# Kernel optimization log

Hardware: AMD Instinct MI355X
Metric: run time of the kernel (lower is better)

Reference implementation:

```python
import jax, jax.numpy as jnp
import numpy as np

PAD_H, PAD_W = 13, 17  # padded grid
GRID_H, GRID_W = 11, 15  # real hex grid (165 hexes)


def _build_convinds() -> np.ndarray:
    """Flat indices into the (13*17,) padded grid of the 7 hex neighbors per cell."""
    off0 = np.array([-17, -16, -1, 0, 1, 17, 18])
    off1 = np.array([-18, -17, -1, 0, 1, 16, 17])
    inds = np.zeros((GRID_H, GRID_W, 7), dtype=np.int32)
    for y in range(1, GRID_H + 1):
        for x in range(1, GRID_W + 1):
            base = y * PAD_W + x
            inds[y - 1, x - 1] = (off0 if y % 2 == 0 else off1) + base
    return inds.reshape(-1)  # (165*7,)


def setup_inputs() -> dict:
    key = jax.random.key(0)
    k1, k2, k3 = jax.random.split(key, 3)
    B, HEXDIM, OUT = 2048, 64, 64
    x = jax.random.normal(k1, (B, 165, HEXDIM), dtype=jnp.float32)
    W = jax.random.normal(k2, (OUT, 7 * HEXDIM), dtype=jnp.float32) * 0.05
    bias = jax.random.normal(k3, (OUT,), dtype=jnp.float32) * 0.05
    return {"x": x, "W": W, "bias": bias}


def reference(x, W, bias):
    convinds = jnp.asarray(_build_convinds())  # static (1155,)
    b, _, hexdim = x.shape
    xg = x.reshape(b, GRID_H, GRID_W, hexdim)
    padded = jnp.zeros((b, PAD_H, PAD_W, hexdim), dtype=x.dtype)
    padded = padded.at[:, 1:GRID_H + 1, 1:GRID_W + 1, :].set(xg)
    padded = padded.reshape(b, PAD_H * PAD_W, hexdim)
    # gather 7 neighbors per hex -> (b, 165, 7*hexdim)
    fc_in = padded[:, convinds, :].reshape(b, 165, 7 * hexdim)
    return jnp.einsum('bnk,ok->bno', fc_in, W) + bias
```

## Files before the change

kernel.cpp:

```cpp
#include <hip/hip_runtime.h>
#include <stdint.h>

typedef __bf16 bf16x8 __attribute__((ext_vector_type(8)));
typedef float floatx4 __attribute__((ext_vector_type(4)));
typedef uint32_t uint32x4 __attribute__((ext_vector_type(4)));

#define GRID_W   15
#define PAD_W    17
#define CELLS    221
#define HEXDIM   64
#define NHEX     165
#define OUTC     64
#define KDIM     448
#define CWORDS   32
#define SXWORDS  (CELLS * CWORDS)
#define SPB      4
#define XF4      (NHEX * HEXDIM / 4)

__device__ __forceinline__ uint32_t pack2bf(float a, float b) {
    union { float f; uint32_t u; } ua, ub;
    ua.f = a; ub.f = b;
    uint32_t ra = (ua.u + 0x7fffu + ((ua.u >> 16) & 1u)) >> 16;
    uint32_t rb = (ub.u + 0x7fffu + ((ub.u >> 16) & 1u)) >> 16;
    return ra | (rb << 16);
}

__global__ void wprep_kernel(const float* __restrict__ W, uint32_t* __restrict__ Wbf) {
    int i = blockIdx.x * 256 + threadIdx.x;
    float4 v = ((const float4*)W)[i];
    uint2 p; p.x = pack2bf(v.x, v.y); p.y = pack2bf(v.z, v.w);
    ((uint2*)Wbf)[i] = p;
}

__device__ __forceinline__ floatx4 mfma16(uint32x4 a, uint32x4 b, floatx4 c) {
    return __builtin_amdgcn_mfma_f32_16x16x32_bf16(
        __builtin_bit_cast(bf16x8, a), __builtin_bit_cast(bf16x8, b), c, 0, 0, 0);
}

template<int HALF>
__device__ __forceinline__ void compute_half(const uint32_t* __restrict__ sb,
                                             const uint32_t* __restrict__ w0,
                                             const uint32_t* __restrict__ w1,
                                             const int* base3, const int* use3,
                                             const int* valid3, int kq, int mg,
                                             floatx4 acc[3][2])
{
    const int off0[7] = {-17, -16, -1, 0, 1, 17, 18};
    const int off1[7] = {-18, -17, -1, 0, 1, 16, 17};
    #pragma unroll
    for (int ksl = 0; ksl < 7; ++ksl) {
        uint32x4 wfa = *(const uint32x4*)(w0 + HALF * 112 + ksl * 16);
        uint32x4 wfb = *(const uint32x4*)(w1 + HALF * 112 + ksl * 16);
        const int ks = HALF * 7 + ksl;
        const int j  = ks >> 1;
        const int h  = ks & 1;
        #pragma unroll
        for (int mt3 = 0; mt3 < 3; ++mt3) {
            if ((mg * 3 + mt3) * 16 < NHEX) {
                int c  = valid3[mt3] ? (base3[mt3] + (use3[mt3] ? off0[j] : off1[j]))
                                     : 16;
                int ch = ((h * 4 + kq) ^ (c & 7));
                uint32x4 bv = *(const uint32x4*)(sb + c * CWORDS + ch * 4);
                acc[mt3][0] = mfma16(wfa, bv, acc[mt3][0]);
                acc[mt3][1] = mfma16(wfb, bv, acc[mt3][1]);
            }
        }
    }
}

__global__ __launch_bounds__(512, 2)
void hexconv_kernel(const float* __restrict__ x,
                    const uint32_t* __restrict__ Wbf,
                    const float* __restrict__ bias,
                    float* __restrict__ out, int B)
{
    __shared__ __align__(16) uint32_t sx[2 * SXWORDS];

    const int tid  = threadIdx.x;
    const int wave = tid >> 6;
    const int lane = tid & 63;
    const int col  = lane & 15;
    const int kq   = lane >> 4;
    const int og   = wave & 1;
    const int mg   = wave >> 1;

    const uint32_t* w0 = Wbf + (og * 32 + col) * (KDIM / 2) + kq * 4;
    const uint32_t* w1 = w0 + 16 * (KDIM / 2);

    int dstoff[6];
    #pragma unroll
    for (int j = 0; j < 6; ++j) {
        int i  = tid + j * 512;
        int ii = (i < XF4) ? i : 0;
        int n = ii >> 4, d = ii & 15;
        int y0 = n / GRID_W, x0 = n - y0 * GRID_W;
        int cell = (y0 + 1) * PAD_W + (x0 + 1);
        int pc   = (d >> 1) ^ (cell & 7);
        dstoff[j] = cell * CWORDS + pc * 4 + (d & 1) * 2;
    }

    const int s0 = blockIdx.x * SPB;
    const float4* xs0 = (const float4*)x + (size_t)s0 * XF4;

    {
        float4 pv[6];
        if (s0 < B) {
            #pragma unroll
            for (int j = 0; j < 5; ++j) pv[j] = xs0[tid + j * 512];
            if (tid < XF4 - 5 * 512) pv[5] = xs0[tid + 5 * 512];
        }
        if (tid < 56 * 8) {
            int c = tid >> 3, ch = tid & 7;
            int cell;
            if (c < 17)      cell = c;
            else if (c < 34) cell = 12 * PAD_W + (c - 17);
            else if (c < 45) cell = (c - 33) * PAD_W;
            else             cell = (c - 44) * PAD_W + 16;
            uint32x4 z = {0u, 0u, 0u, 0u};
            *(uint32x4*)(sx + cell * CWORDS + ch * 4) = z;
            *(uint32x4*)(sx + SXWORDS + cell * CWORDS + ch * 4) = z;
        }
        if (s0 < B) {
            #pragma unroll
            for (int j = 0; j < 5; ++j) {
                uint2 p; p.x = pack2bf(pv[j].x, pv[j].y); p.y = pack2bf(pv[j].z, pv[j].w);
                *(uint2*)(sx + dstoff[j]) = p;
            }
            if (tid < XF4 - 5 * 512) {
                uint2 p; p.x = pack2bf(pv[5].x, pv[5].y); p.y = pack2bf(pv[5].z, pv[5].w);
                *(uint2*)(sx + dstoff[5]) = p;
            }
        }
    }
    __syncthreads();

    #pragma unroll 1
    for (int s = 0; s < SPB; ++s) {
        const int  gs   = s0 + s;
        const bool sval = gs < B;
        const bool nval = (s + 1 < SPB) && (gs + 1 < B);
        const uint32_t* sb = sx + (s & 1) * SXWORDS;

        int base3[3], use3[3], valid3[3];
        floatx4 acc[3][2];
        #pragma unroll
        for (int m = 0; m < 3; ++m) {
            acc[m][0] = (floatx4){0.f, 0.f, 0.f, 0.f};
            acc[m][1] = (floatx4){0.f, 0.f, 0.f, 0.f};
        }

        if (sval) {
            #pragma unroll
            for (int mt3 = 0; mt3 < 3; ++mt3) {
                int mt = mg * 3 + mt3;
                int n  = mt * 16 + col;
                bool valid = (n < NHEX);
                int nn = valid ? n : 0;
                int y0 = nn / GRID_W, x0 = nn - y0 * GRID_W;
                base3[mt3]  = (y0 + 1) * PAD_W + (x0 + 1);
                use3[mt3]   = (y0 & 1);
                valid3[mt3] = valid;
            }
            compute_half<0>(sb, w0, w1, base3, use3, valid3, kq, mg, acc);
        }

        float4 sv[6];
        if (nval) {
            __builtin_amdgcn_sched_barrier(0);
            const float4* xsn = xs0 + (size_t)(s + 1) * XF4;
            #pragma unroll
            for (int j = 0; j < 5; ++j) sv[j] = xsn[tid + j * 512];
            if (tid < XF4 - 5 * 512) sv[5] = xsn[tid + 5 * 512];
            __builtin_amdgcn_sched_barrier(0);
        }

        if (sval) compute_half<1>(sb, w0, w1, base3, use3, valid3, kq, mg, acc);

        if (s + 1 < SPB) {
            if (nval) {
                uint32_t* db = sx + ((s + 1) & 1) * SXWORDS;
                #pragma unroll
                for (int j = 0; j < 5; ++j) {
                    uint2 p; p.x = pack2bf(sv[j].x, sv[j].y); p.y = pack2bf(sv[j].z, sv[j].w);
                    *(uint2*)(db + dstoff[j]) = p;
                }
                if (tid < XF4 - 5 * 512) {
                    uint2 p; p.x = pack2bf(sv[5].x, sv[5].y); p.y = pack2bf(sv[5].z, sv[5].w);
                    *(uint2*)(db + dstoff[5]) = p;
                }
            }
            __syncthreads();
        }

        if (sval) {
            float4 b40 = *(const float4*)(bias + og * 32 + kq * 4);
            float4 b41 = *(const float4*)(bias + og * 32 + 16 + kq * 4);
            float* outb = out + (size_t)gs * NHEX * OUTC;
            #pragma unroll
            for (int mt3 = 0; mt3 < 3; ++mt3) {
                int n = (mg * 3 + mt3) * 16 + col;
                if (n < NHEX) {
                    float* po = outb + (size_t)n * OUTC + og * 32 + kq * 4;
                    float4 v0, v1;
                    v0.x = acc[mt3][0][0] + b40.x; v0.y = acc[mt3][0][1] + b40.y;
                    v0.z = acc[mt3][0][2] + b40.z; v0.w = acc[mt3][0][3] + b40.w;
                    v1.x = acc[mt3][1][0] + b41.x; v1.y = acc[mt3][1][1] + b41.y;
                    v1.z = acc[mt3][1][2] + b41.z; v1.w = acc[mt3][1][3] + b41.w;
                    *(float4*)po        = v0;
                    *(float4*)(po + 16) = v1;
                }
            }
        }
    }
}

extern "C" void kernel_launch(void* const* d_in, const int* in_sizes, int n_in,
                              void* d_out, int out_size, void* d_ws, size_t ws_size,
                              hipStream_t stream) {
    const float* x    = (const float*)d_in[0];
    const float* W    = (const float*)d_in[1];
    const float* bias = (const float*)d_in[2];
    float* out        = (float*)d_out;
    uint32_t* Wbf     = (uint32_t*)d_ws;

    wprep_kernel<<<28, 256, 0, stream>>>(W, Wbf);

    int B = in_sizes[0] / (NHEX * HEXDIM);
    int nb = (B + SPB - 1) / SPB;
    hexconv_kernel<<<nb, 512, 0, stream>>>(x, Wbf, bias, out, B);
}
```

Measured before the change: 210.6 us.

## Pipeline hex conv over half-channel units with padded smem stride

Splits each sample's 64 input channels into two 32-channel halves that are staged and double-buffered separately in LDS, using a padded cell stride of 20 words instead of an XOR swizzle over 32. The weights are reordered in the prep kernel to match the half-channel K ordering. Samples per block drop from 4 to 2, giving twice as many blocks. Smaller LDS buffers and finer-grained units are meant to raise occupancy and overlap global loads with MFMA work, at the cost of more barriers per sample.

```diff
diff --git a/kernel.cpp b/kernel.cpp
--- a/kernel.cpp
+++ b/kernel.cpp
@@ -12,10 +12,11 @@
 #define NHEX     165
 #define OUTC     64
 #define KDIM     448
-#define CWORDS   32
-#define SXWORDS  (CELLS * CWORDS)
-#define SPB      4
-#define XF4      (NHEX * HEXDIM / 4)
+#define CSTRIDE  20
+#define HBWORDS  (CELLS * CSTRIDE)
+#define SPB      2
+#define NUNITS   (2 * SPB)
+#define HF4      (NHEX * 8)
 
 __device__ __forceinline__ uint32_t pack2bf(float a, float b) {
     union { float f; uint32_t u; } ua, ub;
@@ -26,46 +27,19 @@
 }
 
 __global__ void wprep_kernel(const float* __restrict__ W, uint32_t* __restrict__ Wbf) {
-    int i = blockIdx.x * 256 + threadIdx.x;
-    float4 v = ((const float4*)W)[i];
-    uint2 p; p.x = pack2bf(v.x, v.y); p.y = pack2bf(v.z, v.w);
-    ((uint2*)Wbf)[i] = p;
+    int o = blockIdx.x;
+    int r = threadIdx.x;
+    if (r < 224) {
+        int H = r / 112, rr = r - H * 112;
+        int j = rr >> 4, w = rr & 15;
+        const float* src = W + o * KDIM + j * 64 + H * 32 + w * 2;
+        Wbf[o * 224 + r] = pack2bf(src[0], src[1]);
+    }
 }
 
 __device__ __forceinline__ floatx4 mfma16(uint32x4 a, uint32x4 b, floatx4 c) {
     return __builtin_amdgcn_mfma_f32_16x16x32_bf16(
         __builtin_bit_cast(bf16x8, a), __builtin_bit_cast(bf16x8, b), c, 0, 0, 0);
-}
-
-template<int HALF>
-__device__ __forceinline__ void compute_half(const uint32_t* __restrict__ sb,
-                                             const uint32_t* __restrict__ w0,
-                                             const uint32_t* __restrict__ w1,
-                                             const int* base3, const int* use3,
-                                             const int* valid3, int kq, int mg,
-                                             floatx4 acc[3][2])
-{
-    const int off0[7] = {-17, -16, -1, 0, 1, 17, 18};
-    const int off1[7] = {-18, -17, -1, 0, 1, 16, 17};
-    #pragma unroll
-    for (int ksl = 0; ksl < 7; ++ksl) {
-        uint32x4 wfa = *(const uint32x4*)(w0 + HALF * 112 + ksl * 16);
-        uint32x4 wfb = *(const uint32x4*)(w1 + HALF * 112 + ksl * 16);
-        const int ks = HALF * 7 + ksl;
-        const int j  = ks >> 1;
-        const int h  = ks & 1;
-        #pragma unroll
-        for (int mt3 = 0; mt3 < 3; ++mt3) {
-            if ((mg * 3 + mt3) * 16 < NHEX) {
-                int c  = valid3[mt3] ? (base3[mt3] + (use3[mt3] ? off0[j] : off1[j]))
-                                     : 16;
-                int ch = ((h * 4 + kq) ^ (c & 7));
-                uint32x4 bv = *(const uint32x4*)(sb + c * CWORDS + ch * 4);
-                acc[mt3][0] = mfma16(wfa, bv, acc[mt3][0]);
-                acc[mt3][1] = mfma16(wfb, bv, acc[mt3][1]);
-            }
-        }
-    }
 }
 
 __global__ __launch_bounds__(512, 2)
@@ -74,7 +48,7 @@
                     const float* __restrict__ bias,
                     float* __restrict__ out, int B)
 {
-    __shared__ __align__(16) uint32_t sx[2 * SXWORDS];
+    __shared__ __align__(16) uint32_t sx[2 * HBWORDS];
 
     const int tid  = threadIdx.x;
     const int wave = tid >> 6;
@@ -84,130 +58,148 @@
     const int og   = wave & 1;
     const int mg   = wave >> 1;
 
-    const uint32_t* w0 = Wbf + (og * 32 + col) * (KDIM / 2) + kq * 4;
-    const uint32_t* w1 = w0 + 16 * (KDIM / 2);
-
-    int dstoff[6];
+    const uint32_t* w0 = Wbf + (og * 32 + col) * 224 + kq * 4;
+    const uint32_t* w1 = w0 + 16 * 224;
+
+    int soff[3], doff[3];
     #pragma unroll
-    for (int j = 0; j < 6; ++j) {
+    for (int j = 0; j < 3; ++j) {
         int i  = tid + j * 512;
-        int ii = (i < XF4) ? i : 0;
-        int n = ii >> 4, d = ii & 15;
+        int ii = (i < HF4) ? i : 0;
+        int n = ii >> 3, dh = ii & 7;
         int y0 = n / GRID_W, x0 = n - y0 * GRID_W;
         int cell = (y0 + 1) * PAD_W + (x0 + 1);
-        int pc   = (d >> 1) ^ (cell & 7);
-        dstoff[j] = cell * CWORDS + pc * 4 + (d & 1) * 2;
+        soff[j] = n * 16 + dh;
+        doff[j] = cell * CSTRIDE + dh * 2;
+    }
+    const bool v2 = tid < (HF4 - 2 * 512);
+
+    const int off0[7] = {-17, -16, -1, 0, 1, 17, 18};
+    const int off1[7] = {-18, -17, -1, 0, 1, 16, 17};
+    int base3[3], use3[3], valid3[3];
+    #pragma unroll
+    for (int mt3 = 0; mt3 < 3; ++mt3) {
+        int n = (mg * 3 + mt3) * 16 + col;
+        bool valid = (n < NHEX);
+        int nn = valid ? n : 0;
+        int y0 = nn / GRID_W, x0 = nn - y0 * GRID_W;
+        base3[mt3]  = (y0 + 1) * PAD_W + (x0 + 1);
+        use3[mt3]   = (y0 & 1);
+        valid3[mt3] = valid;
     }
 
     const int s0 = blockIdx.x * SPB;
-    const float4* xs0 = (const float4*)x + (size_t)s0 * XF4;
+    const float4* xb = (const float4*)(x + (size_t)s0 * NHEX * HEXDIM);
 
     {
-        float4 pv[6];
+        float4 pv0, pv1, pv2;
         if (s0 < B) {
-            #pragma unroll
-            for (int j = 0; j < 5; ++j) pv[j] = xs0[tid + j * 512];
-            if (tid < XF4 - 5 * 512) pv[5] = xs0[tid + 5 * 512];
-        }
-        if (tid < 56 * 8) {
-            int c = tid >> 3, ch = tid & 7;
+            pv0 = xb[soff[0]];
+            pv1 = xb[soff[1]];
+            if (v2) pv2 = xb[soff[2]];
+        }
+        if (tid < 448) {
+            int t = tid; int buf = t >= 224; t -= buf * 224;
+            int c = t >> 2, ch = t & 3;
             int cell;
             if (c < 17)      cell = c;
             else if (c < 34) cell = 12 * PAD_W + (c - 17);
             else if (c < 45) cell = (c - 33) * PAD_W;
             else             cell = (c - 44) * PAD_W + 16;
             uint32x4 z = {0u, 0u, 0u, 0u};
-            *(uint32x4*)(sx + cell * CWORDS + ch * 4) = z;
-            *(uint32x4*)(sx + SXWORDS + cell * CWORDS + ch * 4) = z;
+            *(uint32x4*)(sx + buf * HBWORDS + cell * CSTRIDE + ch * 4) = z;
         }
         if (s0 < B) {
+            uint2 p;
+            p.x = pack2bf(pv0.x, pv0.y); p.y = pack2bf(pv0.z, pv0.w);
+            *(uint2*)(sx + doff[0]) = p;
+            p.x = pack2bf(pv1.x, pv1.y); p.y = pack2bf(pv1.z, pv1.w);
+            *(uint2*)(sx + doff[1]) = p;
+            if (v2) {
+                p.x = pack2bf(pv2.x, pv2.y); p.y = pack2bf(pv2.z, pv2.w);
+                *(uint2*)(sx + doff[2]) = p;
+            }
+        }
+    }
+    __syncthreads();
+
+    floatx4 acc[3][2];
+    #pragma unroll 1
+    for (int u = 0; u < NUNITS; ++u) {
+        const int s = u >> 1, H = u & 1;
+        const bool uval = (s0 + s) < B;
+        const bool nval = (u + 1 < NUNITS) && ((s0 + ((u + 1) >> 1)) < B);
+        const uint32_t* sb = sx + H * HBWORDS;
+
+        if (H == 0) {
             #pragma unroll
-            for (int j = 0; j < 5; ++j) {
-                uint2 p; p.x = pack2bf(pv[j].x, pv[j].y); p.y = pack2bf(pv[j].z, pv[j].w);
-                *(uint2*)(sx + dstoff[j]) = p;
-            }
-            if (tid < XF4 - 5 * 512) {
-                uint2 p; p.x = pack2bf(pv[5].x, pv[5].y); p.y = pack2bf(pv[5].z, pv[5].w);
-                *(uint2*)(sx + dstoff[5]) = p;
-            }
-        }
-    }
-    __syncthreads();
-
-    #pragma unroll 1
-    for (int s = 0; s < SPB; ++s) {
-        const int  gs   = s0 + s;
-        const bool sval = gs < B;
-        const bool nval = (s + 1 < SPB) && (gs + 1 < B);
-        const uint32_t* sb = sx + (s & 1) * SXWORDS;
-
-        int base3[3], use3[3], valid3[3];
-        floatx4 acc[3][2];
-        #pragma unroll
-        for (int m = 0; m < 3; ++m) {
-            acc[m][0] = (floatx4){0.f, 0.f, 0.f, 0.f};
-            acc[m][1] = (floatx4){0.f, 0.f, 0.f, 0.f};
-        }
-
-        if (sval) {
+            for (int m = 0; m < 3; ++m) {
+                acc[m][0] = (floatx4){0.f, 0.f, 0.f, 0.f};
+                acc[m][1] = (floatx4){0.f, 0.f, 0.f, 0.f};
+            }
+        }
+
+        float4 sv0, sv1, sv2;
+        if (nval) {
+            const float4* xs = xb + (size_t)((u + 1) >> 1) * (NHEX * HEXDIM / 4);
+            int hb = ((u + 1) & 1) * 8;
+            sv0 = xs[soff[0] + hb];
+            sv1 = xs[soff[1] + hb];
+            if (v2) sv2 = xs[soff[2] + hb];
+            __builtin_amdgcn_sched_barrier(0);
+        }
+
+        if (uval) {
+            const int Hw = H * 112;
             #pragma unroll
-            for (int mt3 = 0; mt3 < 3; ++mt3) {
-                int mt = mg * 3 + mt3;
-                int n  = mt * 16 + col;
-                bool valid = (n < NHEX);
-                int nn = valid ? n : 0;
-                int y0 = nn / GRID_W, x0 = nn - y0 * GRID_W;
-                base3[mt3]  = (y0 + 1) * PAD_W + (x0 + 1);
-                use3[mt3]   = (y0 & 1);
-                valid3[mt3] = valid;
-            }
-            compute_half<0>(sb, w0, w1, base3, use3, valid3, kq, mg, acc);
-        }
-
-        float4 sv[6];
-        if (nval) {
-            __builtin_amdgcn_sched_barrier(0);
-            const float4* xsn = xs0 + (size_t)(s + 1) * XF4;
-            #pragma unroll
-            for (int j = 0; j < 5; ++j) sv[j] = xsn[tid + j * 512];
-            if (tid < XF4 - 5 * 512) sv[5] = xsn[tid + 5 * 512];
-            __builtin_amdgcn_sched_barrier(0);
-        }
-
-        if (sval) compute_half<1>(sb, w0, w1, base3, use3, valid3, kq, mg, acc);
-
-        if (s + 1 < SPB) {
+            for (int j = 0; j < 7; ++j) {
+                uint32x4 wfa = *(const uint32x4*)(w0 + Hw + j * 16);
+                uint32x4 wfb = *(const uint32x4*)(w1 + Hw + j * 16);
+                #pragma unroll
+                for (int mt3 = 0; mt3 < 3; ++mt3) {
+                    if ((mg * 3 + mt3) * 16 < NHEX) {
+                        int c = valid3[mt3] ? (base3[mt3] + (use3[mt3] ? off0[j] : off1[j]))
+                                            : 16;
+                        uint32x4 bv = *(const uint32x4*)(sb + c * CSTRIDE + kq * 4);
+                        acc[mt3][0] = mfma16(wfa, bv, acc[mt3][0]);
+                        acc[mt3][1] = mfma16(wfb, bv, acc[mt3][1]);
+                    }
+                }
+            }
+        }
+
+        if (u + 1 < NUNITS) {
             if (nval) {
-                uint32_t* db = sx + ((s + 1) & 1) * SXWORDS;
-                #pragma unroll
-                for (int j = 0; j < 5; ++j) {
-                    uint2 p; p.x = pack2bf(sv[j].x, sv[j].y); p.y = pack2bf(sv[j].z, sv[j].w);
-                    *(uint2*)(db + dstoff[j]) = p;
+                uint32_t* db = sx + ((u + 1) & 1) * HBWORDS;
+                uint2 p;
+                p.x = pack2bf(sv0.x, sv0.y); p.y = pack2bf(sv0.z, sv0.w);
+                *(uint2*)(db + doff[0]) = p;
+                p.x = pack2bf(sv1.x, sv1.y); p.y = pack2bf(sv1.z, sv1.w);
+                *(uint2*)(db + doff[1]) = p;
+                if (v2) {
+                    p.x = pack2bf(sv2.x, sv2.y); p.y = pack2bf(sv2.z, sv2.w);
+                    *(uint2*)(db + doff[2]) = p;
                 }
-                if (tid < XF4 - 5 * 512) {
-                    uint2 p; p.x = pack2bf(sv[5].x, sv[5].y); p.y = pack2bf(sv[5].z, sv[5].w);
-                    *(uint2*)(db + dstoff[5]) = p;
-                }
             }
             __syncthreads();
         }
 
-        if (sval) {
+        if (H == 1 && uval) {
             float4 b40 = *(const float4*)(bias + og * 32 + kq * 4);
             float4 b41 = *(const float4*)(bias + og * 32 + 16 + kq * 4);
-            float* outb = out + (size_t)gs * NHEX * OUTC;
+            float* outb = out + (size_t)(s0 + s) * NHEX * OUTC;
             #pragma unroll
             for (int mt3 = 0; mt3 < 3; ++mt3) {
                 int n = (mg * 3 + mt3) * 16 + col;
                 if (n < NHEX) {
                     float* po = outb + (size_t)n * OUTC + og * 32 + kq * 4;
-                    float4 v0, v1;
-                    v0.x = acc[mt3][0][0] + b40.x; v0.y = acc[mt3][0][1] + b40.y;
-                    v0.z = acc[mt3][0][2] + b40.z; v0.w = acc[mt3][0][3] + b40.w;
-                    v1.x = acc[mt3][1][0] + b41.x; v1.y = acc[mt3][1][1] + b41.y;
-                    v1.z = acc[mt3][1][2] + b41.z; v1.w = acc[mt3][1][3] + b41.w;
-                    *(float4*)po        = v0;
-                    *(float4*)(po + 16) = v1;
+                    float4 o0, o1;
+                    o0.x = acc[mt3][0][0] + b40.x; o0.y = acc[mt3][0][1] + b40.y;
+                    o0.z = acc[mt3][0][2] + b40.z; o0.w = acc[mt3][0][3] + b40.w;
+                    o1.x = acc[mt3][1][0] + b41.x; o1.y = acc[mt3][1][1] + b41.y;
+                    o1.z = acc[mt3][1][2] + b41.z; o1.w = acc[mt3][1][3] + b41.w;
+                    *(float4*)po        = o0;
+                    *(float4*)(po + 16) = o1;
                 }
             }
         }
@@ -223,7 +215,7 @@
     float* out        = (float*)d_out;
     uint32_t* Wbf     = (uint32_t*)d_ws;
 
-    wprep_kernel<<<28, 256, 0, stream>>>(W, Wbf);
+    wprep_kernel<<<64, 256, 0, stream>>>(W, Wbf);
 
     int B = in_sizes[0] / (NHEX * HEXDIM);
     int nb = (B + SPB - 1) / SPB;
```

Result: faster. 203.0 us (-3.6%).
